# Kernel tuning notes

Measured on AMD Instinct MI355X. Metric: run time of the kernel, lower is better.

## Reference

```python
import jax, jax.numpy as jnp
import numpy as np

HEADS = 8
GROUPS = 8  # min(8, ch)
EPS = 1e-5


def group_norm(x, gamma, beta):
    # x: (B, C, H, W); normalize over (C/G, H, W) per group
    B, C, H, W = x.shape
    xg = x.reshape(B, GROUPS, C // GROUPS, H, W)
    mu = jnp.mean(xg, axis=(2, 3, 4), keepdims=True)
    var = jnp.var(xg, axis=(2, 3, 4), keepdims=True)
    xn = ((xg - mu) * jax.lax.rsqrt(var + EPS)).reshape(B, C, H, W)
    return xn * gamma[None, :, None, None] + beta[None, :, None, None]


def setup_inputs() -> dict:
    key = jax.random.key(0)
    k1, k2, k3 = jax.random.split(key, 3)
    B, C, H, W = 8, 512, 32, 32
    x = jax.random.normal(k1, (B, C, H, W), dtype=jnp.float32)
    gn_gamma = jnp.ones((C,), dtype=jnp.float32)
    gn_beta = jnp.zeros((C,), dtype=jnp.float32)
    # conv1x1 weights, torch shape (out,in,1,1) squeezed to (out,in)
    w_qkv = jax.random.normal(k2, (3 * C, C), dtype=jnp.float32) * (1.0 / np.sqrt(C))
    w_proj = jax.random.normal(k3, (C, C), dtype=jnp.float32) * (1.0 / np.sqrt(C))
    b_proj = jnp.zeros((C,), dtype=jnp.float32)
    return {"x": x, "gn_gamma": gn_gamma, "gn_beta": gn_beta,
            "w_qkv": w_qkv, "w_proj": w_proj, "b_proj": b_proj}


def reference(x, gn_gamma, gn_beta, w_qkv, w_proj, b_proj):
    B, C, H, W = x.shape
    hd = C // HEADS  # head_dim
    N = H * W
    xn = group_norm(x, gn_gamma, gn_beta)
    # 1x1 conv == channel matmul: (B,3C,H,W)
    qkv = jnp.einsum('oc,bchw->bohw', w_qkv, xn)
    q, k, v = jnp.split(qkv, 3, axis=1)

    def sh(t):  # (B,C,H,W) -> (B, heads, N, head_dim)
        return t.reshape(B, HEADS, hd, N).transpose(0, 1, 3, 2)

    q, k, v = sh(q), sh(k), sh(v)
    scale = hd ** -0.5
    attn = jax.nn.softmax(jnp.einsum('bhnd,bhmd->bhnm', q, k) * scale, axis=-1)
    out = jnp.einsum('bhnm,bhmd->bhnd', attn, v)  # (B,heads,N,hd)
    out = out.transpose(0, 1, 3, 2).reshape(B, C, H, W)
    proj = jnp.einsum('oc,bchw->bohw', w_proj, out) + b_proj[None, :, None, None]
    return x + proj
```

## Files before the change

### kernel.cpp

```cpp
#include <hip/hip_runtime.h>
#include <cstdint>


typedef __bf16 bf16_t;
typedef bf16_t bf16x8 __attribute__((ext_vector_type(8)));
typedef float f32x4 __attribute__((ext_vector_type(4)));

__device__ __forceinline__ uint16_t f2bf(float f) {
  uint32_t x = __builtin_bit_cast(uint32_t, f);
  x += 0x7FFFu + ((x >> 16) & 1u);
  return (uint16_t)(x >> 16);
}
__device__ __forceinline__ bf16x8 frag_ld(const uint16_t* p) {
  return __builtin_bit_cast(bf16x8, *(const uint4*)p);
}
__device__ __forceinline__ void gl_lds16(const uint16_t* g, uint16_t* l) {
  __builtin_amdgcn_global_load_lds(
      (const __attribute__((address_space(1))) uint32_t*)g,
      (__attribute__((address_space(3))) uint32_t*)l, 16, 0, 0);
}
#define MFMA16(a, b, c) __builtin_amdgcn_mfma_f32_16x16x32_bf16((a), (b), (c), 0, 0, 0)

__global__ __launch_bounds__(256) void prep_k(const float* __restrict__ wq,
                                              const float* __restrict__ wp,
                                              uint16_t* __restrict__ wqb,
                                              uint16_t* __restrict__ wpb,
                                              const float* __restrict__ x,
                                              float* __restrict__ stats) {
  __shared__ alignas(16) float r1[256];
  __shared__ alignas(16) float r2[256];
  int bx = blockIdx.x, t = threadIdx.x;
  if (bx < 512) {
    int idx = (bx * 256 + t) * 8;
    const float* s;
    uint16_t* d;
    if (idx < 786432) { s = wq + idx; d = wqb + idx; }
    else              { s = wp + (idx - 786432); d = wpb + (idx - 786432); }
    float4 a = *(const float4*)s;
    float4 b = *(const float4*)(s + 4);
    union { uint16_t u[8]; uint4 v; } o;
    o.u[0] = f2bf(a.x); o.u[1] = f2bf(a.y); o.u[2] = f2bf(a.z); o.u[3] = f2bf(a.w);
    o.u[4] = f2bf(b.x); o.u[5] = f2bf(b.y); o.u[6] = f2bf(b.z); o.u[7] = f2bf(b.w);
    *(uint4*)d = o.v;
    return;
  }
  int bg = bx - 512;
  const float4* p4 = (const float4*)(x + (size_t)bg * 65536);
  float s1 = 0.f, s2 = 0.f;
  for (int i = t; i < 16384; i += 256) {
    float4 u = p4[i];
    s1 += u.x + u.y + u.z + u.w;
    s2 += u.x * u.x + u.y * u.y + u.z * u.z + u.w * u.w;
  }
  r1[t] = s1; r2[t] = s2; __syncthreads();
  for (int o = 128; o > 0; o >>= 1) {
    if (t < o) { r1[t] += r1[t + o]; r2[t] += r2[t + o]; }
    __syncthreads();
  }
  if (t == 0) {
    float mu = r1[0] * (1.0f / 65536.0f);
    float var = r2[0] * (1.0f / 65536.0f) - mu * mu;
    stats[bg * 2] = mu;
    stats[bg * 2 + 1] = rsqrtf(var + 1e-5f);
  }
}

__global__ __launch_bounds__(256) void gn_apply_k(const float* __restrict__ x,
                                                  const float* __restrict__ gamma,
                                                  const float* __restrict__ beta,
                                                  const float* __restrict__ stats,
                                                  uint16_t* __restrict__ xn) {
  int nt = blockIdx.x, g = blockIdx.y, b = blockIdx.z;
  int n0 = nt * 64;
  float mu   = stats[(b * 8 + g) * 2];
  float rstd = stats[(b * 8 + g) * 2 + 1];
  __shared__ alignas(16) uint16_t tile[64][72];
  int t = threadIdx.x;
  {
    int c_loc = t >> 2;
    int nch = (t & 3) * 16;
    int c = g * 64 + c_loc;
    float gm = gamma[c], bt = beta[c];
    const float* src = x + (size_t)b * 524288 + (size_t)c * 1024 + n0 + nch;
#pragma unroll
    for (int hh = 0; hh < 2; hh++) {
      float4 u0 = *(const float4*)(src + hh * 8);
      float4 u1 = *(const float4*)(src + hh * 8 + 4);
      union { uint16_t u16[8]; uint4 v; } o;
      o.u16[0] = f2bf((u0.x - mu) * rstd * gm + bt);
      o.u16[1] = f2bf((u0.y - mu) * rstd * gm + bt);
      o.u16[2] = f2bf((u0.z - mu) * rstd * gm + bt);
      o.u16[3] = f2bf((u0.w - mu) * rstd * gm + bt);
      o.u16[4] = f2bf((u1.x - mu) * rstd * gm + bt);
      o.u16[5] = f2bf((u1.y - mu) * rstd * gm + bt);
      o.u16[6] = f2bf((u1.z - mu) * rstd * gm + bt);
      o.u16[7] = f2bf((u1.w - mu) * rstd * gm + bt);
      *(uint4*)&tile[c_loc][nch + hh * 8] = o.v;
    }
  }
  __syncthreads();
  {
    int n_loc = t >> 2;
    int c0 = (t & 3) * 16;
    union { uint16_t u16[16]; uint4 v[2]; } o;
#pragma unroll
    for (int j = 0; j < 16; j++) o.u16[j] = tile[c0 + j][n_loc];
    uint16_t* dst = xn + (size_t)b * 524288 + (size_t)(n0 + n_loc) * 512 + g * 64 + c0;
    *(uint4*)dst = o.v[0];
    *(uint4*)(dst + 8) = o.v[1];
  }
}

template <int MODE>
__device__ __forceinline__ void gemm_body(uint16_t* Sh,
                                          const uint16_t* Arow, const uint16_t* Brow,
                                          const float* xres, const float* biasf,
                                          uint16_t* O0, uint16_t* O1, float* Of,
                                          int b, int n0, int o0) {
  uint16_t* As = Sh;
  uint16_t* Bs = Sh + 8192;
  int t = threadIdx.x;
  int lane = t & 63, w = t >> 6;
  int qd = lane >> 4, l15 = lane & 15;
  int wm = w & 1, wn = w >> 1;

  const uint16_t* gA[4];
  const uint16_t* gB[4];
  uint16_t* lA[4];
  uint16_t* lB[4];
#pragma unroll
  for (int i = 0; i < 4; i++) {
    int p = i * 256 + t;
    int row = p >> 3, slot = p & 7, gc = slot ^ (row & 7);
    gA[i] = Arow + (size_t)row * 512 + gc * 8;
    gB[i] = Brow + (size_t)row * 512 + gc * 8;
    lA[i] = As + (size_t)(p - lane) * 8;
    lB[i] = Bs + (size_t)(p - lane) * 8;
  }

  f32x4 acc[4][4] = {};

  for (int k0 = 0; k0 < 512; k0 += 64) {
    __syncthreads();
#pragma unroll
    for (int i = 0; i < 4; i++) { gl_lds16(gA[i] + k0, lA[i]); gl_lds16(gB[i] + k0, lB[i]); }
    __syncthreads();

#pragma unroll
    for (int h = 0; h < 2; h++) {
      int slot = (h * 4 + qd) ^ (l15 & 7);
      bf16x8 af[4], bfr[4];
#pragma unroll
      for (int mt = 0; mt < 4; mt++)
        af[mt] = frag_ld(As + (size_t)(wm * 64 + mt * 16 + l15) * 64 + slot * 8);
#pragma unroll
      for (int nt2 = 0; nt2 < 4; nt2++)
        bfr[nt2] = frag_ld(Bs + (size_t)(wn * 64 + nt2 * 16 + l15) * 64 + slot * 8);
#pragma unroll
      for (int mt = 0; mt < 4; mt++)
#pragma unroll
        for (int nt2 = 0; nt2 < 4; nt2++)
          acc[mt][nt2] = MFMA16(af[mt], bfr[nt2], acc[mt][nt2]);
    }
  }

  if constexpr (MODE == 2) {
#pragma unroll
    for (int mt = 0; mt < 4; mt++) {
      int row = wm * 64 + mt * 16 + qd * 4;
#pragma unroll
      for (int nt2 = 0; nt2 < 4; nt2++) {
        int col = wn * 64 + nt2 * 16 + l15;
#pragma unroll
        for (int r = 0; r < 4; r++) {
          int orow = o0 + row + r, n = n0 + col;
          size_t idx = (size_t)b * 524288 + (size_t)orow * 1024 + n;
          Of[idx] = xres[idx] + biasf[orow] + acc[mt][nt2][r];
        }
      }
    }
  } else {
    __syncthreads();
    uint16_t* buf = Sh + w * 1152;
    float sc = 1.0f;
    uint16_t* gbase;
    size_t rstride;
    int coff;
    if constexpr (MODE == 0) {
      int oc = o0 + wn * 64;
      int hh;
      uint16_t* db;
      if (oc < 512) { db = O0; hh = oc >> 6; sc = 0.125f; }
      else          { db = O1; hh = (oc - 512) >> 6; }
      gbase = db + (size_t)(b * 8 + hh) * 65536 + (size_t)(n0 + wm * 64) * 64;
      rstride = 64;  coff = 0;
    } else {
      gbase = O0 + (size_t)b * 524288 + (size_t)(o0 + wm * 64) * 1024;
      rstride = 1024; coff = n0 + wn * 64;
    }
    int jrow = lane >> 3, joff = (lane & 7) * 8;
#pragma unroll
    for (int mt = 0; mt < 4; mt++) {
#pragma unroll
      for (int nt2 = 0; nt2 < 4; nt2++)
#pragma unroll
        for (int r = 0; r < 4; r++)
          buf[(qd * 4 + r) * 72 + nt2 * 16 + l15] = f2bf(acc[mt][nt2][r] * sc);
#pragma unroll
      for (int half = 0; half < 2; half++) {
        int row = jrow + half * 8;
        uint4 v = *(const uint4*)(buf + row * 72 + joff);
        *(uint4*)(gbase + (size_t)(mt * 16 + row) * rstride + coff + joff) = v;
      }
    }
  }
}

__global__ __launch_bounds__(256) void gemm01_k(const uint16_t* __restrict__ xn,
                                                const uint16_t* __restrict__ wqb,
                                                uint16_t* __restrict__ qtw,
                                                uint16_t* __restrict__ ktw,
                                                uint16_t* __restrict__ vtw) {
  __shared__ alignas(16) uint16_t Sh[16384];
  int bn = blockIdx.y;
  int b = bn >> 3, n0 = (bn & 7) * 128;
  if (blockIdx.x < 8) {
    int o0 = blockIdx.x * 128;
    gemm_body<0>(Sh, xn + (size_t)b * 524288 + (size_t)n0 * 512,
                 wqb + (size_t)o0 * 512, nullptr, nullptr, qtw, ktw, nullptr, b, n0, o0);
  } else {
    int o0 = (blockIdx.x - 8) * 128;
    gemm_body<1>(Sh, wqb + (size_t)(1024 + o0) * 512,
                 xn + (size_t)b * 524288 + (size_t)n0 * 512, nullptr, nullptr,
                 vtw, nullptr, nullptr, b, n0, o0);
  }
}

__global__ __launch_bounds__(256) void gemm2_k(const uint16_t* __restrict__ wpb,
                                               const uint16_t* __restrict__ otw,
                                               const float* __restrict__ xres,
                                               const float* __restrict__ biasf,
                                               float* __restrict__ out) {
  __shared__ alignas(16) uint16_t Sh[16384];
  int bn = blockIdx.y;
  int b = bn >> 3, n0 = (bn & 7) * 128;
  int o0 = blockIdx.x * 128;
  gemm_body<2>(Sh, wpb + (size_t)o0 * 512,
               otw + (size_t)b * 524288 + (size_t)n0 * 512, xres, biasf,
               nullptr, nullptr, out, b, n0, o0);
}

__global__ __launch_bounds__(256) void attn_k(const uint16_t* __restrict__ qt,
                                              const uint16_t* __restrict__ ktp,
                                              const uint16_t* __restrict__ vtp,
                                              uint16_t* __restrict__ ot) {
  int bh = blockIdx.x;
  int b = bh >> 3, h = bh & 7;
  int n0 = blockIdx.y * 128;
  const uint16_t* qbase = qt + (size_t)bh * 65536;
  const uint16_t* kbase = ktp + (size_t)bh * 65536;
  const uint16_t* vbase = vtp + (size_t)b * 524288 + (size_t)h * 65536;

  __shared__ alignas(16) uint16_t Ks[2][64 * 64];
  __shared__ alignas(16) uint16_t Vs[2][64 * 64];
  __shared__ alignas(16) uint16_t Ps[128 * 72];

  int t = threadIdx.x, lane = t & 63, w = t >> 6;
  int qd = lane >> 4, l15 = lane & 15;

  bf16x8 qf[2][2];
#pragma unroll
  for (int rs = 0; rs < 2; rs++) {
    const uint16_t* qp = qbase + (size_t)(n0 + w * 32 + rs * 16 + l15) * 64 + qd * 8;
    qf[rs][0] = frag_ld(qp);
    qf[rs][1] = frag_ld(qp + 32);
  }

  int p1 = t, p2 = t + 256;
  int r1 = p1 >> 3, gc1 = (p1 & 7) ^ (r1 & 7);
  int r2 = p2 >> 3, gc2 = (p2 & 7) ^ (r2 & 7);
  const uint16_t* gK1 = kbase + (size_t)r1 * 64 + gc1 * 8;
  const uint16_t* gK2 = kbase + (size_t)r2 * 64 + gc2 * 8;
  const uint16_t* gV1 = vbase + (size_t)r1 * 1024 + gc1 * 8;
  const uint16_t* gV2 = vbase + (size_t)r2 * 1024 + gc2 * 8;
  int lo1 = (p1 - lane) * 8;
  int lo2 = (p2 - lane) * 8;

  f32x4 oaccT[2][4] = {};
  float lsum[2] = {0.f, 0.f};

  gl_lds16(gK1, &Ks[0][lo1]);
  gl_lds16(gK2, &Ks[0][lo2]);
  gl_lds16(gV1, &Vs[0][lo1]);
  gl_lds16(gV2, &Vs[0][lo2]);
  __syncthreads();

  for (int it = 0; it < 16; it++) {
    int cur = it & 1, nxt = cur ^ 1;
    if (it < 15) {
      int m0 = (it + 1) * 64;
      gl_lds16(gK1 + (size_t)m0 * 64, &Ks[nxt][lo1]);
      gl_lds16(gK2 + (size_t)m0 * 64, &Ks[nxt][lo2]);
      gl_lds16(gV1 + m0, &Vs[nxt][lo1]);
      gl_lds16(gV2 + m0, &Vs[nxt][lo2]);
    }
    const uint16_t* Kc = Ks[cur];
    const uint16_t* Vc = Vs[cur];

    f32x4 sacc[2][4] = {};
#pragma unroll
    for (int mt = 0; mt < 4; mt++) {
      int row = mt * 16 + l15;
      int s0 = qd ^ (l15 & 7);
      bf16x8 kf0 = frag_ld(Kc + (size_t)row * 64 + s0 * 8);
      bf16x8 kf1 = frag_ld(Kc + (size_t)row * 64 + (s0 ^ 4) * 8);
#pragma unroll
      for (int rs = 0; rs < 2; rs++) {
        sacc[rs][mt] = MFMA16(kf0, qf[rs][0], sacc[rs][mt]);
        sacc[rs][mt] = MFMA16(kf1, qf[rs][1], sacc[rs][mt]);
      }
    }

#pragma unroll
    for (int rs = 0; rs < 2; rs++)
#pragma unroll
      for (int mt = 0; mt < 4; mt++) {
        union { uint16_t u[4]; uint2 v; } pk;
        float psum = 0.f;
#pragma unroll
        for (int r = 0; r < 4; r++) {
          float p = __expf(sacc[rs][mt][r]);
          psum += p;
          pk.u[r] = (uint16_t)(__builtin_bit_cast(uint32_t, p) >> 16);
        }
        lsum[rs] += psum;
        *(uint2*)(Ps + (size_t)(w * 32 + rs * 16 + l15) * 72 + mt * 16 + qd * 4) = pk.v;
      }

    bf16x8 pf[2][2];
#pragma unroll
    for (int rs = 0; rs < 2; rs++)
#pragma unroll
      for (int ks = 0; ks < 2; ks++)
        pf[rs][ks] = frag_ld(Ps + (size_t)(w * 32 + rs * 16 + l15) * 72 + ks * 32 + qd * 8);
#pragma unroll
    for (int dt = 0; dt < 4; dt++)
#pragma unroll
      for (int ks = 0; ks < 2; ks++) {
        int row = dt * 16 + l15;
        int slot = (ks * 4 + qd) ^ (l15 & 7);
        bf16x8 vf = frag_ld(Vc + (size_t)row * 64 + slot * 8);
#pragma unroll
        for (int rs = 0; rs < 2; rs++)
          oaccT[rs][dt] = MFMA16(vf, pf[rs][ks], oaccT[rs][dt]);
      }

    __syncthreads();
  }

#pragma unroll
  for (int rs = 0; rs < 2; rs++) {
    float s = lsum[rs];
    s += __shfl_xor(s, 16);
    s += __shfl_xor(s, 32);
    float rinv = 1.0f / s;
    int n = n0 + w * 32 + rs * 16 + l15;
    uint16_t* orow = ot + (size_t)b * 524288 + (size_t)n * 512 + h * 64;
#pragma unroll
    for (int dt = 0; dt < 4; dt++) {
      union { uint16_t u[4]; uint2 v; } pk;
#pragma unroll
      for (int r = 0; r < 4; r++) pk.u[r] = f2bf(oaccT[rs][dt][r] * rinv);
      *(uint2*)(orow + dt * 16 + qd * 4) = pk.v;
    }
  }
}

extern "C" void kernel_launch(void* const* d_in, const int* in_sizes, int n_in,
                              void* d_out, int out_size, void* d_ws, size_t ws_size,
                              hipStream_t stream) {
  (void)in_sizes; (void)n_in; (void)out_size; (void)ws_size;
  const float* xf   = (const float*)d_in[0];
  const float* gamf = (const float*)d_in[1];
  const float* betf = (const float*)d_in[2];
  const float* wqf  = (const float*)d_in[3];
  const float* wpf  = (const float*)d_in[4];
  const float* bprf = (const float*)d_in[5];
  float* out = (float*)d_out;

  uint16_t* base = (uint16_t*)d_ws;
  float* stats   = (float*)base;
  uint16_t* wqb  = base + 512;
  uint16_t* wpb  = wqb + 786432;
  uint16_t* xn   = wpb + 262144;
  uint16_t* qtw  = xn  + 4194304;
  uint16_t* ktw  = qtw + 4194304;
  uint16_t* vtw  = ktw + 4194304;
  uint16_t* otw  = xn;

  prep_k<<<576, 256, 0, stream>>>(wqf, wpf, wqb, wpb, xf, stats);
  gn_apply_k<<<dim3(16, 8, 8), 256, 0, stream>>>(xf, gamf, betf, stats, xn);
  gemm01_k<<<dim3(12, 64), 256, 0, stream>>>(xn, wqb, qtw, ktw, vtw);
  attn_k<<<dim3(64, 8), 256, 0, stream>>>(qtw, ktw, vtw, otw);
  gemm2_k<<<dim3(4, 64), 256, 0, stream>>>(wpb, otw, xf, bprf, out);
}
```

Before: 174.2 us.

## Fuse group-norm stats and apply, double-buffer output projection GEMM

The group-norm statistics and the normalize/transpose pass now run in one kernel. Each of 64 blocks reduces its group and then streams all 16 column tiles itself, which removes a launch and the stats round trip. The price is only 64 blocks doing the apply work instead of 1024, so that phase has far less parallelism. The projection GEMM gets its own kernel with double-buffered LDS loads overlapping the MFMA work, and both GEMM grids are flattened to 1D with a new block ordering.

```diff
diff --git a/kernel.cpp b/kernel.cpp
--- a/kernel.cpp
+++ b/kernel.cpp
@@ -21,14 +21,18 @@
 }
 #define MFMA16(a, b, c) __builtin_amdgcn_mfma_f32_16x16x32_bf16((a), (b), (c), 0, 0, 0)
 
-__global__ __launch_bounds__(256) void prep_k(const float* __restrict__ wq,
-                                              const float* __restrict__ wp,
-                                              uint16_t* __restrict__ wqb,
-                                              uint16_t* __restrict__ wpb,
-                                              const float* __restrict__ x,
-                                              float* __restrict__ stats) {
+__global__ __launch_bounds__(256) void gnfused_k(const float* __restrict__ wq,
+                                                 const float* __restrict__ wp,
+                                                 uint16_t* __restrict__ wqb,
+                                                 uint16_t* __restrict__ wpb,
+                                                 const float* __restrict__ x,
+                                                 const float* __restrict__ gamma,
+                                                 const float* __restrict__ beta,
+                                                 uint16_t* __restrict__ xn) {
   __shared__ alignas(16) float r1[256];
   __shared__ alignas(16) float r2[256];
+  __shared__ alignas(16) uint16_t tile[64][72];
+  __shared__ float smu, srstd;
   int bx = blockIdx.x, t = threadIdx.x;
   if (bx < 512) {
     int idx = (bx * 256 + t) * 8;
@@ -45,77 +49,74 @@
     return;
   }
   int bg = bx - 512;
-  const float4* p4 = (const float4*)(x + (size_t)bg * 65536);
-  float s1 = 0.f, s2 = 0.f;
-  for (int i = t; i < 16384; i += 256) {
-    float4 u = p4[i];
-    s1 += u.x + u.y + u.z + u.w;
-    s2 += u.x * u.x + u.y * u.y + u.z * u.z + u.w * u.w;
-  }
-  r1[t] = s1; r2[t] = s2; __syncthreads();
-  for (int o = 128; o > 0; o >>= 1) {
-    if (t < o) { r1[t] += r1[t + o]; r2[t] += r2[t + o]; }
-    __syncthreads();
-  }
-  if (t == 0) {
-    float mu = r1[0] * (1.0f / 65536.0f);
-    float var = r2[0] * (1.0f / 65536.0f) - mu * mu;
-    stats[bg * 2] = mu;
-    stats[bg * 2 + 1] = rsqrtf(var + 1e-5f);
-  }
-}
-
-__global__ __launch_bounds__(256) void gn_apply_k(const float* __restrict__ x,
-                                                  const float* __restrict__ gamma,
-                                                  const float* __restrict__ beta,
-                                                  const float* __restrict__ stats,
-                                                  uint16_t* __restrict__ xn) {
-  int nt = blockIdx.x, g = blockIdx.y, b = blockIdx.z;
-  int n0 = nt * 64;
-  float mu   = stats[(b * 8 + g) * 2];
-  float rstd = stats[(b * 8 + g) * 2 + 1];
-  __shared__ alignas(16) uint16_t tile[64][72];
-  int t = threadIdx.x;
+  int b = bg >> 3, g = bg & 7;
+  const float* xbase = x + (size_t)bg * 65536;
+
   {
-    int c_loc = t >> 2;
-    int nch = (t & 3) * 16;
-    int c = g * 64 + c_loc;
-    float gm = gamma[c], bt = beta[c];
-    const float* src = x + (size_t)b * 524288 + (size_t)c * 1024 + n0 + nch;
-#pragma unroll
-    for (int hh = 0; hh < 2; hh++) {
-      float4 u0 = *(const float4*)(src + hh * 8);
-      float4 u1 = *(const float4*)(src + hh * 8 + 4);
-      union { uint16_t u16[8]; uint4 v; } o;
-      o.u16[0] = f2bf((u0.x - mu) * rstd * gm + bt);
-      o.u16[1] = f2bf((u0.y - mu) * rstd * gm + bt);
-      o.u16[2] = f2bf((u0.z - mu) * rstd * gm + bt);
-      o.u16[3] = f2bf((u0.w - mu) * rstd * gm + bt);
-      o.u16[4] = f2bf((u1.x - mu) * rstd * gm + bt);
-      o.u16[5] = f2bf((u1.y - mu) * rstd * gm + bt);
-      o.u16[6] = f2bf((u1.z - mu) * rstd * gm + bt);
-      o.u16[7] = f2bf((u1.w - mu) * rstd * gm + bt);
-      *(uint4*)&tile[c_loc][nch + hh * 8] = o.v;
-    }
-  }
-  __syncthreads();
-  {
-    int n_loc = t >> 2;
-    int c0 = (t & 3) * 16;
-    union { uint16_t u16[16]; uint4 v[2]; } o;
-#pragma unroll
-    for (int j = 0; j < 16; j++) o.u16[j] = tile[c0 + j][n_loc];
-    uint16_t* dst = xn + (size_t)b * 524288 + (size_t)(n0 + n_loc) * 512 + g * 64 + c0;
-    *(uint4*)dst = o.v[0];
-    *(uint4*)(dst + 8) = o.v[1];
+    const float4* p4 = (const float4*)xbase;
+    float s1 = 0.f, s2 = 0.f;
+    for (int i = t; i < 16384; i += 256) {
+      float4 u = p4[i];
+      s1 += u.x + u.y + u.z + u.w;
+      s2 += u.x * u.x + u.y * u.y + u.z * u.z + u.w * u.w;
+    }
+    r1[t] = s1; r2[t] = s2; __syncthreads();
+    for (int o = 128; o > 0; o >>= 1) {
+      if (t < o) { r1[t] += r1[t + o]; r2[t] += r2[t + o]; }
+      __syncthreads();
+    }
+    if (t == 0) {
+      float mu = r1[0] * (1.0f / 65536.0f);
+      float var = r2[0] * (1.0f / 65536.0f) - mu * mu;
+      smu = mu; srstd = rsqrtf(var + 1e-5f);
+    }
+    __syncthreads();
+  }
+  float mu = smu, rstd = srstd;
+
+  int c_loc = t >> 2, nch = (t & 3) * 16;
+  int c = g * 64 + c_loc;
+  float gm = gamma[c], bt = beta[c];
+  const float* srcc = xbase + (size_t)c_loc * 1024;
+  int n_loc = t >> 2, c0 = (t & 3) * 16;
+  uint16_t* dstc = xn + (size_t)b * 524288 + g * 64 + c0;
+  for (int nt = 0; nt < 16; nt++) {
+    int n0 = nt * 64;
+    {
+      const float* src = srcc + n0 + nch;
+#pragma unroll
+      for (int hh = 0; hh < 2; hh++) {
+        float4 u0 = *(const float4*)(src + hh * 8);
+        float4 u1 = *(const float4*)(src + hh * 8 + 4);
+        union { uint16_t u16[8]; uint4 v; } o;
+        o.u16[0] = f2bf((u0.x - mu) * rstd * gm + bt);
+        o.u16[1] = f2bf((u0.y - mu) * rstd * gm + bt);
+        o.u16[2] = f2bf((u0.z - mu) * rstd * gm + bt);
+        o.u16[3] = f2bf((u0.w - mu) * rstd * gm + bt);
+        o.u16[4] = f2bf((u1.x - mu) * rstd * gm + bt);
+        o.u16[5] = f2bf((u1.y - mu) * rstd * gm + bt);
+        o.u16[6] = f2bf((u1.z - mu) * rstd * gm + bt);
+        o.u16[7] = f2bf((u1.w - mu) * rstd * gm + bt);
+        *(uint4*)&tile[c_loc][nch + hh * 8] = o.v;
+      }
+    }
+    __syncthreads();
+    {
+      union { uint16_t u16[16]; uint4 v[2]; } o;
+#pragma unroll
+      for (int j = 0; j < 16; j++) o.u16[j] = tile[c0 + j][n_loc];
+      uint16_t* dst = dstc + (size_t)(n0 + n_loc) * 512;
+      *(uint4*)dst = o.v[0];
+      *(uint4*)(dst + 8) = o.v[1];
+    }
+    __syncthreads();
   }
 }
 
 template <int MODE>
 __device__ __forceinline__ void gemm_body(uint16_t* Sh,
                                           const uint16_t* Arow, const uint16_t* Brow,
-                                          const float* xres, const float* biasf,
-                                          uint16_t* O0, uint16_t* O1, float* Of,
+                                          uint16_t* O0, uint16_t* O1,
                                           int b, int n0, int o0) {
   uint16_t* As = Sh;
   uint16_t* Bs = Sh + 8192;
@@ -152,10 +153,10 @@
       bf16x8 af[4], bfr[4];
 #pragma unroll
       for (int mt = 0; mt < 4; mt++)
-        af[mt] = frag_ld(As + (size_t)(wm * 64 + mt * 16 + l15) * 64 + slot * 8);
+        af[mt] = frag_ld(As + (wm * 64 + mt * 16 + l15) * 64 + slot * 8);
 #pragma unroll
       for (int nt2 = 0; nt2 < 4; nt2++)
-        bfr[nt2] = frag_ld(Bs + (size_t)(wn * 64 + nt2 * 16 + l15) * 64 + slot * 8);
+        bfr[nt2] = frag_ld(Bs + (wn * 64 + nt2 * 16 + l15) * 64 + slot * 8);
 #pragma unroll
       for (int mt = 0; mt < 4; mt++)
 #pragma unroll
@@ -164,54 +165,37 @@
     }
   }
 
-  if constexpr (MODE == 2) {
-#pragma unroll
-    for (int mt = 0; mt < 4; mt++) {
-      int row = wm * 64 + mt * 16 + qd * 4;
-#pragma unroll
-      for (int nt2 = 0; nt2 < 4; nt2++) {
-        int col = wn * 64 + nt2 * 16 + l15;
-#pragma unroll
-        for (int r = 0; r < 4; r++) {
-          int orow = o0 + row + r, n = n0 + col;
-          size_t idx = (size_t)b * 524288 + (size_t)orow * 1024 + n;
-          Of[idx] = xres[idx] + biasf[orow] + acc[mt][nt2][r];
-        }
-      }
-    }
+  __syncthreads();
+  uint16_t* buf = Sh + w * 1152;
+  float sc = 1.0f;
+  uint16_t* gbase;
+  size_t rstride;
+  int coff;
+  if constexpr (MODE == 0) {
+    int oc = o0 + wn * 64;
+    int hh;
+    uint16_t* db;
+    if (oc < 512) { db = O0; hh = oc >> 6; sc = 0.125f; }
+    else          { db = O1; hh = (oc - 512) >> 6; }
+    gbase = db + (size_t)(b * 8 + hh) * 65536 + (size_t)(n0 + wm * 64) * 64;
+    rstride = 64;  coff = 0;
   } else {
-    __syncthreads();
-    uint16_t* buf = Sh + w * 1152;
-    float sc = 1.0f;
-    uint16_t* gbase;
-    size_t rstride;
-    int coff;
-    if constexpr (MODE == 0) {
-      int oc = o0 + wn * 64;
-      int hh;
-      uint16_t* db;
-      if (oc < 512) { db = O0; hh = oc >> 6; sc = 0.125f; }
-      else          { db = O1; hh = (oc - 512) >> 6; }
-      gbase = db + (size_t)(b * 8 + hh) * 65536 + (size_t)(n0 + wm * 64) * 64;
-      rstride = 64;  coff = 0;
-    } else {
-      gbase = O0 + (size_t)b * 524288 + (size_t)(o0 + wm * 64) * 1024;
-      rstride = 1024; coff = n0 + wn * 64;
-    }
-    int jrow = lane >> 3, joff = (lane & 7) * 8;
-#pragma unroll
-    for (int mt = 0; mt < 4; mt++) {
-#pragma unroll
-      for (int nt2 = 0; nt2 < 4; nt2++)
-#pragma unroll
-        for (int r = 0; r < 4; r++)
-          buf[(qd * 4 + r) * 72 + nt2 * 16 + l15] = f2bf(acc[mt][nt2][r] * sc);
-#pragma unroll
-      for (int half = 0; half < 2; half++) {
-        int row = jrow + half * 8;
-        uint4 v = *(const uint4*)(buf + row * 72 + joff);
-        *(uint4*)(gbase + (size_t)(mt * 16 + row) * rstride + coff + joff) = v;
-      }
+    gbase = O0 + (size_t)b * 524288 + (size_t)(o0 + wm * 64) * 1024;
+    rstride = 1024; coff = n0 + wn * 64;
+  }
+  int jrow = lane >> 3, joff = (lane & 7) * 8;
+#pragma unroll
+  for (int mt = 0; mt < 4; mt++) {
+#pragma unroll
+    for (int nt2 = 0; nt2 < 4; nt2++)
+#pragma unroll
+      for (int r = 0; r < 4; r++)
+        buf[(qd * 4 + r) * 72 + nt2 * 16 + l15] = f2bf(acc[mt][nt2][r] * sc);
+#pragma unroll
+    for (int half = 0; half < 2; half++) {
+      int row = jrow + half * 8;
+      uint4 v = *(const uint4*)(buf + row * 72 + joff);
+      *(uint4*)(gbase + (size_t)(mt * 16 + row) * rstride + coff + joff) = v;
     }
   }
 }
@@ -222,17 +206,18 @@
                                                 uint16_t* __restrict__ ktw,
                                                 uint16_t* __restrict__ vtw) {
   __shared__ alignas(16) uint16_t Sh[16384];
-  int bn = blockIdx.y;
-  int b = bn >> 3, n0 = (bn & 7) * 128;
-  if (blockIdx.x < 8) {
-    int o0 = blockIdx.x * 128;
+  int id = blockIdx.x;
+  int lo = id & 7, hi = id >> 3;
+  int o12 = hi % 12, b = hi / 12;
+  int n0 = lo * 128;
+  if (o12 < 8) {
+    int o0 = o12 * 128;
     gemm_body<0>(Sh, xn + (size_t)b * 524288 + (size_t)n0 * 512,
-                 wqb + (size_t)o0 * 512, nullptr, nullptr, qtw, ktw, nullptr, b, n0, o0);
+                 wqb + (size_t)o0 * 512, qtw, ktw, b, n0, o0);
   } else {
-    int o0 = (blockIdx.x - 8) * 128;
+    int o0 = (o12 - 8) * 128;
     gemm_body<1>(Sh, wqb + (size_t)(1024 + o0) * 512,
-                 xn + (size_t)b * 524288 + (size_t)n0 * 512, nullptr, nullptr,
-                 vtw, nullptr, nullptr, b, n0, o0);
+                 xn + (size_t)b * 524288 + (size_t)n0 * 512, vtw, nullptr, b, n0, o0);
   }
 }
 
@@ -241,13 +226,75 @@
                                                const float* __restrict__ xres,
                                                const float* __restrict__ biasf,
                                                float* __restrict__ out) {
-  __shared__ alignas(16) uint16_t Sh[16384];
-  int bn = blockIdx.y;
-  int b = bn >> 3, n0 = (bn & 7) * 128;
-  int o0 = blockIdx.x * 128;
-  gemm_body<2>(Sh, wpb + (size_t)o0 * 512,
-               otw + (size_t)b * 524288 + (size_t)n0 * 512, xres, biasf,
-               nullptr, nullptr, out, b, n0, o0);
+  __shared__ alignas(16) uint16_t As[2][8192];
+  __shared__ alignas(16) uint16_t Bs[2][8192];
+  int id = blockIdx.x;
+  int lo = id & 7, hi = id >> 3;
+  int o0 = (hi & 3) * 128, b = hi >> 2, n0 = lo * 128;
+  const uint16_t* Arow = wpb + (size_t)o0 * 512;
+  const uint16_t* Brow = otw + (size_t)b * 524288 + (size_t)n0 * 512;
+
+  int t = threadIdx.x, lane = t & 63, w = t >> 6;
+  int qd = lane >> 4, l15 = lane & 15;
+  int wm = w & 1, wn = w >> 1;
+
+  const uint16_t* gA[4];
+  const uint16_t* gB[4];
+  int lofs[4];
+#pragma unroll
+  for (int i = 0; i < 4; i++) {
+    int p = i * 256 + t;
+    int row = p >> 3, slot = p & 7, gc = slot ^ (row & 7);
+    gA[i] = Arow + (size_t)row * 512 + gc * 8;
+    gB[i] = Brow + (size_t)row * 512 + gc * 8;
+    lofs[i] = (p - lane) * 8;
+  }
+
+  f32x4 acc[4][4] = {};
+#pragma unroll
+  for (int i = 0; i < 4; i++) { gl_lds16(gA[i], &As[0][lofs[i]]); gl_lds16(gB[i], &Bs[0][lofs[i]]); }
+  __syncthreads();
+
+  for (int kt = 0; kt < 8; kt++) {
+    int cur = kt & 1, nxt = cur ^ 1;
+    if (kt < 7) {
+      int k0 = (kt + 1) * 64;
+#pragma unroll
+      for (int i = 0; i < 4; i++) { gl_lds16(gA[i] + k0, &As[nxt][lofs[i]]); gl_lds16(gB[i] + k0, &Bs[nxt][lofs[i]]); }
+    }
+#pragma unroll
+    for (int h = 0; h < 2; h++) {
+      int slot = (h * 4 + qd) ^ (l15 & 7);
+      bf16x8 af[4], bfr[4];
+#pragma unroll
+      for (int mt = 0; mt < 4; mt++)
+        af[mt] = frag_ld(&As[cur][(wm * 64 + mt * 16 + l15) * 64 + slot * 8]);
+#pragma unroll
+      for (int nt2 = 0; nt2 < 4; nt2++)
+        bfr[nt2] = frag_ld(&Bs[cur][(wn * 64 + nt2 * 16 + l15) * 64 + slot * 8]);
+#pragma unroll
+      for (int mt = 0; mt < 4; mt++)
+#pragma unroll
+        for (int nt2 = 0; nt2 < 4; nt2++)
+          acc[mt][nt2] = MFMA16(af[mt], bfr[nt2], acc[mt][nt2]);
+    }
+    __syncthreads();
+  }
+
+#pragma unroll
+  for (int mt = 0; mt < 4; mt++) {
+    int row = wm * 64 + mt * 16 + qd * 4;
+#pragma unroll
+    for (int nt2 = 0; nt2 < 4; nt2++) {
+      int col = wn * 64 + nt2 * 16 + l15;
+#pragma unroll
+      for (int r = 0; r < 4; r++) {
+        int orow = o0 + row + r, n = n0 + col;
+        size_t idx = (size_t)b * 524288 + (size_t)orow * 1024 + n;
+        out[idx] = xres[idx] + biasf[orow] + acc[mt][nt2][r];
+      }
+    }
+  }
 }
 
 __global__ __launch_bounds__(256) void attn_k(const uint16_t* __restrict__ qt,
@@ -389,8 +436,7 @@
   float* out = (float*)d_out;
 
   uint16_t* base = (uint16_t*)d_ws;
-  float* stats   = (float*)base;
-  uint16_t* wqb  = base + 512;
+  uint16_t* wqb  = base;
   uint16_t* wpb  = wqb + 786432;
   uint16_t* xn   = wpb + 262144;
   uint16_t* qtw  = xn  + 4194304;
@@ -398,9 +444,8 @@
   uint16_t* vtw  = ktw + 4194304;
   uint16_t* otw  = xn;
 
-  prep_k<<<576, 256, 0, stream>>>(wqf, wpf, wqb, wpb, xf, stats);
-  gn_apply_k<<<dim3(16, 8, 8), 256, 0, stream>>>(xf, gamf, betf, stats, xn);
-  gemm01_k<<<dim3(12, 64), 256, 0, stream>>>(xn, wqb, qtw, ktw, vtw);
+  gnfused_k<<<576, 256, 0, stream>>>(wqf, wpf, wqb, wpb, xf, gamf, betf, xn);
+  gemm01_k<<<768, 256, 0, stream>>>(xn, wqb, qtw, ktw, vtw);
   attn_k<<<dim3(64, 8), 256, 0, stream>>>(qtw, ktw, vtw, otw);
-  gemm2_k<<<dim3(4, 64), 256, 0, stream>>>(wpb, otw, xf, bprf, out);
-}
+  gemm2_k<<<256, 256, 0, stream>>>(wpb, otw, xf, bprf, out);
+}
```

Result: faster. 168.7 us (-3.2%).
